# Optimization experiments

Measured on AMD Instinct MI355X. Metric: run time of the kernel, lower is better.

## Reference

```python
import jax, jax.numpy as jnp
import numpy as np

HEADS = 4  # from init_kwargs

def _branch_index(seq_len: int) -> jnp.ndarray:
    # position 0 -> layer_s(0), 1 -> layer_r(1), 2 -> layer_o(2),
    # then alternating layer_a(3)/layer_v(4) starting at position 3.
    tail = jnp.where((jnp.arange(seq_len - 3) % 2) == 0, 3, 4)
    return jnp.concatenate([jnp.array([0, 1, 2], dtype=tail.dtype), tail])


def setup_inputs() -> dict:
    key = jax.random.key(0)
    k1, k2, k3 = jax.random.split(key, 3)
    B, S, H = 128, 513, 256
    x = jax.random.normal(k1, (B, S, H), dtype=jnp.float32)
    # 5 Linear layers, nn.Linear convention: y = x @ W.T + b, W: [out,in]
    W = jax.random.normal(k2, (5, H, H), dtype=jnp.float32) * (1.0 / np.sqrt(H))
    b = jax.random.normal(k3, (5, H), dtype=jnp.float32) * 0.02
    return {"x": x, "W": W, "b": b}


def reference(x, W, b):
    # Original applies each Linear to a position-masked copy of x and sums.
    # Since the 5 masks are disjoint one-hots over positions, the weight term
    # at position t is x[t] @ W[m(t)].T; the bias term is sum of ALL 5 biases
    # (Linear(0) = bias), applied at every position.
    B, S, H = x.shape
    idx = _branch_index(S)            # [S] in {0..4}
    Wsel = W[idx]
    out = jnp.einsum('bsh,sdh->bsd', x, Wsel) + b.sum(axis=0)
    return out.reshape(B, S, HEADS, H // HEADS)
```

## Files before the change

### kernel.cpp

```cpp
#include <hip/hip_runtime.h>
#include <hip/hip_bf16.h>

#define B_ 128
#define S_ 513
#define H_ 256
#define SH_ (S_ * H_)

typedef __attribute__((ext_vector_type(8))) short short8;
typedef __attribute__((ext_vector_type(4))) float f32x4;

static __device__ inline short8 pack8(float4 a, float4 b) {
    union { short8 s; __hip_bfloat162 h[4]; } u;
    u.h[0] = __float22bfloat162_rn(make_float2(a.x, a.y));
    u.h[1] = __float22bfloat162_rn(make_float2(a.z, a.w));
    u.h[2] = __float22bfloat162_rn(make_float2(b.x, b.y));
    u.h[3] = __float22bfloat162_rn(make_float2(b.z, b.w));
    return u.s;
}

__global__ void prep_kernel(const float* __restrict__ W,
                            const float* __restrict__ bias,
                            unsigned short* __restrict__ Wbf,
                            float* __restrict__ bsum) {
    int t = blockIdx.x * 256 + threadIdx.x;
    if (t < 5 * 32 * 256) {
        int m  = t >> 13;
        int r  = t & 8191;
        int d  = r >> 5;
        int kc = r & 31;
        const float* src = W + (((size_t)m * 256 + d) * 256 + kc * 8);
        float4 v0 = *(const float4*)src;
        float4 v1 = *(const float4*)(src + 4);
        *(short8*)(Wbf + ((size_t)(m * 32 + kc) * 256 + d) * 8) = pack8(v0, v1);
    }
    if (t < H_) {
        float s = 0.f;
#pragma unroll
        for (int i = 0; i < 5; ++i) s += bias[i * H_ + t];
        bsum[t] = s;
    }
}

template <int MODE>
__global__ __launch_bounds__(256, 4)
void sel_gemm_kernel(const float* __restrict__ x,
                     const void* __restrict__ Wp,
                     const void* __restrict__ bp,
                     float* __restrict__ out) {
    const int s     = blockIdx.x >> 1;
    const int bhalf = blockIdx.x & 1;
    const int m_idx = (s < 3) ? s : ((s & 1) ? 3 : 4);

    __shared__ unsigned short As[64 * 256];

    const int t    = threadIdx.x;
    const int lane = t & 63;
    const int w    = t >> 6;
    const int lrow = lane & 15;
    const int quad = lane >> 4;

    const float* xs = x + (size_t)s * H_ + (size_t)bhalf * 64 * SH_;
#pragma unroll
    for (int i = 0; i < 8; ++i) {
        int flat = i * 256 + t;
        int r = flat >> 5;
        int c = flat & 31;
        const float* src = xs + (size_t)r * SH_ + c * 8;
        float4 v0 = *(const float4*)src;
        float4 v1 = *(const float4*)(src + 4);
        *(short8*)&As[r * 256 + ((c ^ (r & 7)) * 8)] = pack8(v0, v1);
    }

    f32x4 acc[4][4];
#pragma unroll
    for (int i = 0; i < 4; ++i)
#pragma unroll
        for (int j = 0; j < 4; ++j) {
            f32x4 z = {0.f, 0.f, 0.f, 0.f};
            acc[i][j] = z;
        }

    __syncthreads();

#pragma unroll
    for (int kk = 0; kk < 8; ++kk) {
        short8 wfr[4];
        if (MODE == 0) {
            const unsigned short* Wk =
                (const unsigned short*)Wp +
                ((size_t)(m_idx * 32 + kk * 4 + quad) * 256) * 8;
#pragma unroll
            for (int j = 0; j < 4; ++j)
                wfr[j] = *(const short8*)(Wk + (size_t)(w * 64 + j * 16 + lrow) * 8);
        } else {
            const float* Wb = (const float*)Wp + (size_t)m_idx * H_ * H_;
#pragma unroll
            for (int j = 0; j < 4; ++j) {
                const float* wrow = Wb + (size_t)(w * 64 + j * 16 + lrow) * H_
                                    + kk * 32 + quad * 8;
                float4 v0 = *(const float4*)wrow;
                float4 v1 = *(const float4*)(wrow + 4);
                wfr[j] = pack8(v0, v1);
            }
        }

        short8 xfr[4];
        const int cc = kk * 4 + quad;
#pragma unroll
        for (int i = 0; i < 4; ++i) {
            int r = i * 16 + lrow;
            xfr[i] = *(const short8*)&As[r * 256 + ((cc ^ (r & 7)) * 8)];
        }

#pragma unroll
        for (int j = 0; j < 4; ++j)
#pragma unroll
            for (int i = 0; i < 4; ++i)
                acc[i][j] = __builtin_amdgcn_mfma_f32_16x16x32_bf16(
                    wfr[j], xfr[i], acc[i][j], 0, 0, 0);
    }

#pragma unroll
    for (int j = 0; j < 4; ++j) {
        const int d0 = w * 64 + j * 16 + quad * 4;
        f32x4 bj;
        if (MODE == 0) {
            bj = *(const f32x4*)((const float*)bp + d0);
        } else {
            const float* bias = (const float*)bp;
#pragma unroll
            for (int r = 0; r < 4; ++r) {
                float sum = 0.f;
#pragma unroll
                for (int i = 0; i < 5; ++i) sum += bias[i * H_ + d0 + r];
                bj[r] = sum;
            }
        }
#pragma unroll
        for (int i = 0; i < 4; ++i) {
            const int b = bhalf * 64 + i * 16 + lrow;
            f32x4 v = acc[i][j] + bj;
            *(f32x4*)(out + ((size_t)b * S_ + s) * H_ + d0) = v;
        }
    }
}

extern "C" void kernel_launch(void* const* d_in, const int* in_sizes, int n_in,
                              void* d_out, int out_size, void* d_ws, size_t ws_size,
                              hipStream_t stream) {
    const float* x    = (const float*)d_in[0];
    const float* W    = (const float*)d_in[1];
    const float* bias = (const float*)d_in[2];
    float* out = (float*)d_out;

    const size_t w_elems  = (size_t)5 * H_ * H_;
    const size_t ws_need  = w_elems * sizeof(unsigned short) + H_ * sizeof(float);

    if (ws_size >= ws_need) {
        unsigned short* Wbf = (unsigned short*)d_ws;
        float* bsum = (float*)((char*)d_ws + w_elems * sizeof(unsigned short));
        prep_kernel<<<dim3(160), dim3(256), 0, stream>>>(W, bias, Wbf, bsum);
        sel_gemm_kernel<0><<<dim3(2 * S_), dim3(256), 0, stream>>>(
            x, (const void*)Wbf, (const void*)bsum, out);
    } else {
        sel_gemm_kernel<1><<<dim3(2 * S_), dim3(256), 0, stream>>>(
            x, (const void*)W, (const void*)bias, out);
    }
}
```

Baseline: 130.9 us.

## Process all batches per position with double-buffered x tiles in shared memory

Each block now handles one sequence position across all 128 batch rows in four chunks of 32, instead of two blocks each taking 64 rows. The x loads for the next chunk are issued into registers while the current chunk's MFMAs run, then committed to the alternate LDS buffer, so global loads overlap with compute. The bias sums are loaded once per block. The cost is half as many blocks (513 on a 256-CU part), a lower occupancy hint, and W fragments reloaded for each chunk.

After: 144.0 us. 10.0% more time.

```diff
diff --git a/kernel.cpp b/kernel.cpp
--- a/kernel.cpp
+++ b/kernel.cpp
@@ -42,106 +42,138 @@
 }
 
 template <int MODE>
-__global__ __launch_bounds__(256, 4)
+__global__ __launch_bounds__(256, 2)
 void sel_gemm_kernel(const float* __restrict__ x,
                      const void* __restrict__ Wp,
                      const void* __restrict__ bp,
                      float* __restrict__ out) {
-    const int s     = blockIdx.x >> 1;
-    const int bhalf = blockIdx.x & 1;
+    const int s     = blockIdx.x;
     const int m_idx = (s < 3) ? s : ((s & 1) ? 3 : 4);
 
-    __shared__ unsigned short As[64 * 256];
+    __shared__ unsigned short As[2][32 * 256];
 
     const int t    = threadIdx.x;
     const int lane = t & 63;
     const int w    = t >> 6;
     const int lrow = lane & 15;
     const int quad = lane >> 4;
-
-    const float* xs = x + (size_t)s * H_ + (size_t)bhalf * 64 * SH_;
-#pragma unroll
-    for (int i = 0; i < 8; ++i) {
-        int flat = i * 256 + t;
-        int r = flat >> 5;
-        int c = flat & 31;
-        const float* src = xs + (size_t)r * SH_ + c * 8;
-        float4 v0 = *(const float4*)src;
-        float4 v1 = *(const float4*)(src + 4);
-        *(short8*)&As[r * 256 + ((c ^ (r & 7)) * 8)] = pack8(v0, v1);
-    }
-
-    f32x4 acc[4][4];
-#pragma unroll
-    for (int i = 0; i < 4; ++i)
+    const int c    = t & 31;
+    const int rb   = t >> 5;
+
+    const float* xs = x + (size_t)s * H_;
+
+    float4 ld[4][2];
+
+    auto issue = [&](int q) {
+#pragma unroll
+        for (int i = 0; i < 4; ++i) {
+            const int r = i * 8 + rb;
+            const float* src = xs + (size_t)(q * 32 + r) * SH_ + c * 8;
+            ld[i][0] = *(const float4*)src;
+            ld[i][1] = *(const float4*)(src + 4);
+        }
+    };
+    auto commit = [&](int buf) {
+#pragma unroll
+        for (int i = 0; i < 4; ++i) {
+            const int r = i * 8 + rb;
+            *(short8*)&As[buf][r * 256 + ((c ^ (r & 7)) * 8)] =
+                pack8(ld[i][0], ld[i][1]);
+        }
+    };
+
+    f32x4 bj4[4];
+    if (MODE == 0) {
+        const float* bsum = (const float*)bp;
+#pragma unroll
+        for (int j = 0; j < 4; ++j)
+            bj4[j] = *(const f32x4*)(bsum + w * 64 + j * 16 + quad * 4);
+    } else {
+        const float* bias = (const float*)bp;
 #pragma unroll
         for (int j = 0; j < 4; ++j) {
-            f32x4 z = {0.f, 0.f, 0.f, 0.f};
-            acc[i][j] = z;
-        }
-
-    __syncthreads();
-
-#pragma unroll
-    for (int kk = 0; kk < 8; ++kk) {
-        short8 wfr[4];
-        if (MODE == 0) {
-            const unsigned short* Wk =
-                (const unsigned short*)Wp +
-                ((size_t)(m_idx * 32 + kk * 4 + quad) * 256) * 8;
-#pragma unroll
-            for (int j = 0; j < 4; ++j)
-                wfr[j] = *(const short8*)(Wk + (size_t)(w * 64 + j * 16 + lrow) * 8);
-        } else {
-            const float* Wb = (const float*)Wp + (size_t)m_idx * H_ * H_;
-#pragma unroll
-            for (int j = 0; j < 4; ++j) {
-                const float* wrow = Wb + (size_t)(w * 64 + j * 16 + lrow) * H_
-                                    + kk * 32 + quad * 8;
-                float4 v0 = *(const float4*)wrow;
-                float4 v1 = *(const float4*)(wrow + 4);
-                wfr[j] = pack8(v0, v1);
-            }
-        }
-
-        short8 xfr[4];
-        const int cc = kk * 4 + quad;
-#pragma unroll
-        for (int i = 0; i < 4; ++i) {
-            int r = i * 16 + lrow;
-            xfr[i] = *(const short8*)&As[r * 256 + ((cc ^ (r & 7)) * 8)];
-        }
-
-#pragma unroll
-        for (int j = 0; j < 4; ++j)
-#pragma unroll
-            for (int i = 0; i < 4; ++i)
-                acc[i][j] = __builtin_amdgcn_mfma_f32_16x16x32_bf16(
-                    wfr[j], xfr[i], acc[i][j], 0, 0, 0);
-    }
-
-#pragma unroll
-    for (int j = 0; j < 4; ++j) {
-        const int d0 = w * 64 + j * 16 + quad * 4;
-        f32x4 bj;
-        if (MODE == 0) {
-            bj = *(const f32x4*)((const float*)bp + d0);
-        } else {
-            const float* bias = (const float*)bp;
+            const int d0 = w * 64 + j * 16 + quad * 4;
 #pragma unroll
             for (int r = 0; r < 4; ++r) {
                 float sum = 0.f;
 #pragma unroll
                 for (int i = 0; i < 5; ++i) sum += bias[i * H_ + d0 + r];
-                bj[r] = sum;
-            }
-        }
-#pragma unroll
-        for (int i = 0; i < 4; ++i) {
-            const int b = bhalf * 64 + i * 16 + lrow;
-            f32x4 v = acc[i][j] + bj;
-            *(f32x4*)(out + ((size_t)b * S_ + s) * H_ + d0) = v;
-        }
+                bj4[j][r] = sum;
+            }
+        }
+    }
+
+    issue(0);
+    commit(0);
+
+#pragma unroll
+    for (int q = 0; q < 4; ++q) {
+        const int cur = q & 1;
+        __syncthreads();
+        if (q < 3) issue(q + 1);
+
+        f32x4 acc[2][4];
+#pragma unroll
+        for (int i = 0; i < 2; ++i)
+#pragma unroll
+            for (int j = 0; j < 4; ++j) {
+                f32x4 z = {0.f, 0.f, 0.f, 0.f};
+                acc[i][j] = z;
+            }
+
+        const unsigned short* Ab = As[cur];
+
+#pragma unroll
+        for (int kk = 0; kk < 8; ++kk) {
+            short8 wfr[4];
+            if (MODE == 0) {
+                const unsigned short* Wk =
+                    (const unsigned short*)Wp +
+                    ((size_t)(m_idx * 32 + kk * 4 + quad) * 256) * 8;
+#pragma unroll
+                for (int j = 0; j < 4; ++j)
+                    wfr[j] = *(const short8*)(Wk +
+                              (size_t)(w * 64 + j * 16 + lrow) * 8);
+            } else {
+                const float* Wb = (const float*)Wp + (size_t)m_idx * H_ * H_;
+#pragma unroll
+                for (int j = 0; j < 4; ++j) {
+                    const float* wrow = Wb +
+                        (size_t)(w * 64 + j * 16 + lrow) * H_ + kk * 32 + quad * 8;
+                    float4 v0 = *(const float4*)wrow;
+                    float4 v1 = *(const float4*)(wrow + 4);
+                    wfr[j] = pack8(v0, v1);
+                }
+            }
+
+            short8 xfr[2];
+            const int cc = kk * 4 + quad;
+#pragma unroll
+            for (int i = 0; i < 2; ++i) {
+                const int r = i * 16 + lrow;
+                xfr[i] = *(const short8*)&Ab[r * 256 + ((cc ^ (r & 7)) * 8)];
+            }
+
+#pragma unroll
+            for (int j = 0; j < 4; ++j)
+#pragma unroll
+                for (int i = 0; i < 2; ++i)
+                    acc[i][j] = __builtin_amdgcn_mfma_f32_16x16x32_bf16(
+                        wfr[j], xfr[i], acc[i][j], 0, 0, 0);
+        }
+
+#pragma unroll
+        for (int j = 0; j < 4; ++j) {
+            const int d0 = w * 64 + j * 16 + quad * 4;
+#pragma unroll
+            for (int i = 0; i < 2; ++i) {
+                const int b = q * 32 + i * 16 + lrow;
+                f32x4 v = acc[i][j] + bj4[j];
+                *(f32x4*)(out + ((size_t)b * S_ + s) * H_ + d0) = v;
+            }
+        }
+
+        if (q < 3) commit(cur ^ 1);
     }
 }
 
@@ -160,10 +192,10 @@
         unsigned short* Wbf = (unsigned short*)d_ws;
         float* bsum = (float*)((char*)d_ws + w_elems * sizeof(unsigned short));
         prep_kernel<<<dim3(160), dim3(256), 0, stream>>>(W, bias, Wbf, bsum);
-        sel_gemm_kernel<0><<<dim3(2 * S_), dim3(256), 0, stream>>>(
+        sel_gemm_kernel<0><<<dim3(S_), dim3(256), 0, stream>>>(
             x, (const void*)Wbf, (const void*)bsum, out);
     } else {
-        sel_gemm_kernel<1><<<dim3(2 * S_), dim3(256), 0, stream>>>(
+        sel_gemm_kernel<1><<<dim3(S_), dim3(256), 0, stream>>>(
             x, (const void*)W, (const void*)bias, out);
     }
 }
```

## Tile rows by batch and position parity instead of per-position batch halves

Applied to the files above, without the earlier changes.

Rows are now grouped so that each block handles one batch and a strided run of same-parity positions, which share a weight matrix. Previously each block handled one position across 64 batches, so every x row and output row sat a full sequence apart in memory. With the new grouping, each block's rows lie at stride 2 within one batch, which gives more contiguous loads and stores and better locality. The first three positions get six extra blocks, and partial tiles are handled by clamping loads and masking stores, which adds a little wasted compute.

Result: no change. 128.7 us (-1.6%).

```diff
diff --git a/kernel.cpp b/kernel.cpp
--- a/kernel.cpp
+++ b/kernel.cpp
@@ -47,9 +47,29 @@
                      const void* __restrict__ Wp,
                      const void* __restrict__ bp,
                      float* __restrict__ out) {
-    const int s     = blockIdx.x >> 1;
-    const int bhalf = blockIdx.x & 1;
-    const int m_idx = (s < 3) ? s : ((s & 1) ? 3 : 4);
+    const int bid = blockIdx.x;
+    int m_idx, rmax, rowstride;
+    size_t rowbase;
+    if (bid < 1024) {
+        const int b    = bid >> 3;
+        const int sub  = bid & 7;
+        const int par  = sub & 1;
+        const int tile = sub >> 1;
+        const int sbase = (par ? 3 : 4) + tile * 128;
+        m_idx     = par ? 3 : 4;
+        rowbase   = (size_t)b * S_ + sbase;
+        rowstride = 2;
+        rmax      = (512 - sbase) >> 1;
+        if (rmax > 63) rmax = 63;
+    } else {
+        const int e  = bid - 1024;
+        const int s  = e >> 1;
+        const int bh = e & 1;
+        m_idx     = s;
+        rowbase   = (size_t)bh * 64 * S_ + s;
+        rowstride = S_;
+        rmax      = 63;
+    }
 
     __shared__ unsigned short As[64 * 256];
 
@@ -59,13 +79,13 @@
     const int lrow = lane & 15;
     const int quad = lane >> 4;
 
-    const float* xs = x + (size_t)s * H_ + (size_t)bhalf * 64 * SH_;
 #pragma unroll
     for (int i = 0; i < 8; ++i) {
         int flat = i * 256 + t;
         int r = flat >> 5;
         int c = flat & 31;
-        const float* src = xs + (size_t)r * SH_ + c * 8;
+        int rc = r <= rmax ? r : rmax;
+        const float* src = x + (rowbase + (size_t)rowstride * rc) * H_ + c * 8;
         float4 v0 = *(const float4*)src;
         float4 v1 = *(const float4*)(src + 4);
         *(short8*)&As[r * 256 + ((c ^ (r & 7)) * 8)] = pack8(v0, v1);
@@ -138,9 +158,11 @@
         }
 #pragma unroll
         for (int i = 0; i < 4; ++i) {
-            const int b = bhalf * 64 + i * 16 + lrow;
-            f32x4 v = acc[i][j] + bj;
-            *(f32x4*)(out + ((size_t)b * S_ + s) * H_ + d0) = v;
+            const int r = i * 16 + lrow;
+            if (r <= rmax) {
+                f32x4 v = acc[i][j] + bj;
+                *(f32x4*)(out + (rowbase + (size_t)rowstride * r) * H_ + d0) = v;
+            }
         }
     }
 }
@@ -156,14 +178,15 @@
     const size_t w_elems  = (size_t)5 * H_ * H_;
     const size_t ws_need  = w_elems * sizeof(unsigned short) + H_ * sizeof(float);
 
+    const int grid = 1024 + 6;
     if (ws_size >= ws_need) {
         unsigned short* Wbf = (unsigned short*)d_ws;
         float* bsum = (float*)((char*)d_ws + w_elems * sizeof(unsigned short));
         prep_kernel<<<dim3(160), dim3(256), 0, stream>>>(W, bias, Wbf, bsum);
-        sel_gemm_kernel<0><<<dim3(2 * S_), dim3(256), 0, stream>>>(
+        sel_gemm_kernel<0><<<dim3(grid), dim3(256), 0, stream>>>(
             x, (const void*)Wbf, (const void*)bsum, out);
     } else {
-        sel_gemm_kernel<1><<<dim3(2 * S_), dim3(256), 0, stream>>>(
+        sel_gemm_kernel<1><<<dim3(grid), dim3(256), 0, stream>>>(
             x, (const void*)W, (const void*)bias, out);
     }
 }
```

## Use producer warp with async global-to-LDS triple buffering and contiguous row tiles

Applied to the files above, without the earlier changes.

Restructures the selective GEMM so each block handles 64 rows of one batch sharing a weight matrix, strided by 2 along the sequence, instead of one position across 64 batches. A dedicated producer wavefront streams fp32 x tiles into a triple-buffered LDS ring with global_load_lds, while four consumer wavefronts convert to bf16 and run MFMA on 16-row tiles. The aim is better x access locality and overlap of global loads with compute. In exchange it adds an extra wavefront per block, lowers the occupancy target, and converts x to bf16 on every fragment load instead of once per tile.

Result: slower. 141.5 us (+8.1%).

```diff
diff --git a/kernel.cpp b/kernel.cpp
--- a/kernel.cpp
+++ b/kernel.cpp
@@ -15,6 +15,14 @@
     u.h[1] = __float22bfloat162_rn(make_float2(a.z, a.w));
     u.h[2] = __float22bfloat162_rn(make_float2(b.x, b.y));
     u.h[3] = __float22bfloat162_rn(make_float2(b.z, b.w));
+    return u.s;
+}
+static __device__ inline short8 pack8v(f32x4 a, f32x4 b) {
+    union { short8 s; __hip_bfloat162 h[4]; } u;
+    u.h[0] = __float22bfloat162_rn(make_float2(a[0], a[1]));
+    u.h[1] = __float22bfloat162_rn(make_float2(a[2], a[3]));
+    u.h[2] = __float22bfloat162_rn(make_float2(b[0], b[1]));
+    u.h[3] = __float22bfloat162_rn(make_float2(b[2], b[3]));
     return u.s;
 }
 
@@ -42,105 +50,164 @@
 }
 
 template <int MODE>
-__global__ __launch_bounds__(256, 4)
+__global__ __launch_bounds__(320, 3)
 void sel_gemm_kernel(const float* __restrict__ x,
                      const void* __restrict__ Wp,
                      const void* __restrict__ bp,
                      float* __restrict__ out) {
-    const int s     = blockIdx.x >> 1;
-    const int bhalf = blockIdx.x & 1;
-    const int m_idx = (s < 3) ? s : ((s & 1) ? 3 : 4);
-
-    __shared__ unsigned short As[64 * 256];
-
+    __shared__ float As[3][16 * 256];
+
+    const int bid  = blockIdx.x;
     const int t    = threadIdx.x;
     const int lane = t & 63;
-    const int w    = t >> 6;
+    const int w8   = t >> 6;
     const int lrow = lane & 15;
     const int quad = lane >> 4;
 
-    const float* xs = x + (size_t)s * H_ + (size_t)bhalf * 64 * SH_;
-#pragma unroll
-    for (int i = 0; i < 8; ++i) {
-        int flat = i * 256 + t;
-        int r = flat >> 5;
-        int c = flat & 31;
-        const float* src = xs + (size_t)r * SH_ + c * 8;
-        float4 v0 = *(const float4*)src;
-        float4 v1 = *(const float4*)(src + 4);
-        *(short8*)&As[r * 256 + ((c ^ (r & 7)) * 8)] = pack8(v0, v1);
-    }
-
-    f32x4 acc[4][4];
-#pragma unroll
-    for (int i = 0; i < 4; ++i)
-#pragma unroll
-        for (int j = 0; j < 4; ++j) {
-            f32x4 z = {0.f, 0.f, 0.f, 0.f};
-            acc[i][j] = z;
-        }
-
-    __syncthreads();
-
-#pragma unroll
-    for (int kk = 0; kk < 8; ++kk) {
-        short8 wfr[4];
+    int m_idx, rmaxg;
+    size_t xrow0, rstride;
+    if (bid < 6) {
+        const int s  = bid >> 1;
+        const int bh = bid & 1;
+        m_idx   = s;
+        xrow0   = (size_t)(bh * 64) * S_ + s;
+        rstride = S_;
+        rmaxg   = 63;
+    } else {
+        const int mb = bid - 6;
+        const int b   = mb >> 3;
+        const int sub = mb & 7;
+        const int par = sub & 1;
+        const int q   = sub >> 1;
+        m_idx   = par ? 3 : 4;
+        xrow0   = (size_t)b * S_ + (par ? 3 : 4) + q * 128;
+        rstride = 2;
+        rmaxg   = 254 - q * 64;
+        if (rmaxg > 63) rmaxg = 63;
+    }
+
+    const bool producer = (w8 == 4);
+
+    if (producer) {
+#pragma unroll
+        for (int tt = 0; tt < 2; ++tt) {
+#pragma unroll
+            for (int it = 0; it < 16; ++it) {
+                int rg = tt * 16 + it;
+                if (rg > rmaxg) rg = rmaxg;
+                const float* src = x + (xrow0 + rstride * rg) * H_
+                                     + ((lane ^ (it & 7)) << 2);
+                __builtin_amdgcn_global_load_lds(
+                    (const __attribute__((address_space(1))) unsigned int*)src,
+                    (__attribute__((address_space(3))) unsigned int*)
+                        &As[tt][it * 256],
+                    16, 0, 0);
+            }
+        }
+    }
+
+    f32x4 bj4[4];
+    if (!producer) {
         if (MODE == 0) {
-            const unsigned short* Wk =
-                (const unsigned short*)Wp +
-                ((size_t)(m_idx * 32 + kk * 4 + quad) * 256) * 8;
+            const float* bsum = (const float*)bp;
 #pragma unroll
             for (int j = 0; j < 4; ++j)
-                wfr[j] = *(const short8*)(Wk + (size_t)(w * 64 + j * 16 + lrow) * 8);
-        } else {
-            const float* Wb = (const float*)Wp + (size_t)m_idx * H_ * H_;
-#pragma unroll
-            for (int j = 0; j < 4; ++j) {
-                const float* wrow = Wb + (size_t)(w * 64 + j * 16 + lrow) * H_
-                                    + kk * 32 + quad * 8;
-                float4 v0 = *(const float4*)wrow;
-                float4 v1 = *(const float4*)(wrow + 4);
-                wfr[j] = pack8(v0, v1);
-            }
-        }
-
-        short8 xfr[4];
-        const int cc = kk * 4 + quad;
-#pragma unroll
-        for (int i = 0; i < 4; ++i) {
-            int r = i * 16 + lrow;
-            xfr[i] = *(const short8*)&As[r * 256 + ((cc ^ (r & 7)) * 8)];
-        }
-
-#pragma unroll
-        for (int j = 0; j < 4; ++j)
-#pragma unroll
-            for (int i = 0; i < 4; ++i)
-                acc[i][j] = __builtin_amdgcn_mfma_f32_16x16x32_bf16(
-                    wfr[j], xfr[i], acc[i][j], 0, 0, 0);
-    }
-
-#pragma unroll
-    for (int j = 0; j < 4; ++j) {
-        const int d0 = w * 64 + j * 16 + quad * 4;
-        f32x4 bj;
-        if (MODE == 0) {
-            bj = *(const f32x4*)((const float*)bp + d0);
+                bj4[j] = *(const f32x4*)(bsum + w8 * 64 + j * 16 + quad * 4);
         } else {
             const float* bias = (const float*)bp;
 #pragma unroll
-            for (int r = 0; r < 4; ++r) {
-                float sum = 0.f;
-#pragma unroll
-                for (int i = 0; i < 5; ++i) sum += bias[i * H_ + d0 + r];
-                bj[r] = sum;
-            }
-        }
-#pragma unroll
-        for (int i = 0; i < 4; ++i) {
-            const int b = bhalf * 64 + i * 16 + lrow;
-            f32x4 v = acc[i][j] + bj;
-            *(f32x4*)(out + ((size_t)b * S_ + s) * H_ + d0) = v;
+            for (int j = 0; j < 4; ++j) {
+                const int d0 = w8 * 64 + j * 16 + quad * 4;
+#pragma unroll
+                for (int r = 0; r < 4; ++r) {
+                    float sum = 0.f;
+#pragma unroll
+                    for (int i = 0; i < 5; ++i) sum += bias[i * H_ + d0 + r];
+                    bj4[j][r] = sum;
+                }
+            }
+        }
+    }
+
+#pragma unroll
+    for (int tt = 0; tt < 4; ++tt) {
+        if (producer) {
+            if (tt < 3) asm volatile("s_waitcnt vmcnt(16)" ::: "memory");
+            else        asm volatile("s_waitcnt vmcnt(0)"  ::: "memory");
+        }
+        __builtin_amdgcn_s_barrier();
+        __builtin_amdgcn_sched_barrier(0);
+
+        if (producer) {
+            if (tt + 2 < 4) {
+                const int slot = (tt + 2) % 3;
+#pragma unroll
+                for (int it = 0; it < 16; ++it) {
+                    int rg = (tt + 2) * 16 + it;
+                    if (rg > rmaxg) rg = rmaxg;
+                    const float* src = x + (xrow0 + rstride * rg) * H_
+                                         + ((lane ^ (it & 7)) << 2);
+                    __builtin_amdgcn_global_load_lds(
+                        (const __attribute__((address_space(1))) unsigned int*)src,
+                        (__attribute__((address_space(3))) unsigned int*)
+                            &As[slot][it * 256],
+                        16, 0, 0);
+                }
+            }
+        } else {
+            const float* Ab = As[tt % 3];
+            f32x4 acc[4];
+#pragma unroll
+            for (int j = 0; j < 4; ++j) {
+                f32x4 z = {0.f, 0.f, 0.f, 0.f};
+                acc[j] = z;
+            }
+
+#pragma unroll
+            for (int kk = 0; kk < 8; ++kk) {
+                short8 wfr[4];
+                if (MODE == 0) {
+                    const unsigned short* Wk =
+                        (const unsigned short*)Wp +
+                        ((size_t)(m_idx * 32 + kk * 4 + quad) * 256) * 8;
+#pragma unroll
+                    for (int j = 0; j < 4; ++j)
+                        wfr[j] = *(const short8*)(Wk +
+                                  (size_t)(w8 * 64 + j * 16 + lrow) * 8);
+                } else {
+                    const float* Wb = (const float*)Wp + (size_t)m_idx * H_ * H_;
+#pragma unroll
+                    for (int j = 0; j < 4; ++j) {
+                        const float* wrow = Wb +
+                            (size_t)(w8 * 64 + j * 16 + lrow) * H_
+                            + kk * 32 + quad * 8;
+                        float4 v0 = *(const float4*)wrow;
+                        float4 v1 = *(const float4*)(wrow + 4);
+                        wfr[j] = pack8(v0, v1);
+                    }
+                }
+
+                const int g0 = kk * 8 + quad * 2;
+                const int r  = lrow;
+                f32x4 f0 = *(const f32x4*)&Ab[r * 256 + (((g0    ) ^ (r & 7)) << 2)];
+                f32x4 f1 = *(const f32x4*)&Ab[r * 256 + (((g0 + 1) ^ (r & 7)) << 2)];
+                short8 xf = pack8v(f0, f1);
+
+#pragma unroll
+                for (int j = 0; j < 4; ++j)
+                    acc[j] = __builtin_amdgcn_mfma_f32_16x16x32_bf16(
+                        wfr[j], xf, acc[j], 0, 0, 0);
+            }
+
+            const int rg = tt * 16 + lrow;
+            if (rg <= rmaxg) {
+#pragma unroll
+                for (int j = 0; j < 4; ++j) {
+                    const int d0 = w8 * 64 + j * 16 + quad * 4;
+                    f32x4 v = acc[j] + bj4[j];
+                    *(f32x4*)(out + (xrow0 + rstride * rg) * H_ + d0) = v;
+                }
+            }
         }
     }
 }
@@ -156,14 +223,15 @@
     const size_t w_elems  = (size_t)5 * H_ * H_;
     const size_t ws_need  = w_elems * sizeof(unsigned short) + H_ * sizeof(float);
 
+    const int grid = 6 + 1024;
     if (ws_size >= ws_need) {
         unsigned short* Wbf = (unsigned short*)d_ws;
         float* bsum = (float*)((char*)d_ws + w_elems * sizeof(unsigned short));
         prep_kernel<<<dim3(160), dim3(256), 0, stream>>>(W, bias, Wbf, bsum);
-        sel_gemm_kernel<0><<<dim3(2 * S_), dim3(256), 0, stream>>>(
+        sel_gemm_kernel<0><<<dim3(grid), dim3(320), 0, stream>>>(
             x, (const void*)Wbf, (const void*)bsum, out);
     } else {
-        sel_gemm_kernel<1><<<dim3(2 * S_), dim3(256), 0, stream>>>(
+        sel_gemm_kernel<1><<<dim3(grid), dim3(320), 0, stream>>>(
             x, (const void*)W, (const void*)bias, out);
     }
 }
```
